# Optimization experiments

Hardware: AMD Instinct MI355X
Metric: run time of the kernel (lower is better)

Reference implementation:

```python
import jax, jax.numpy as jnp
import numpy as np

N_RAYS = 8192
N_SURF = 2048
EPS = 1e-18  # matches torch zero-denominator patch value


def setup_inputs() -> dict:
    key = jax.random.key(0)
    k1, k2, k3 = jax.random.split(key, 3)
    o = jax.random.normal(k1, (N_RAYS, 3), dtype=jnp.float32)
    d = jax.random.normal(k2, (N_RAYS, 3), dtype=jnp.float32)
    V = jax.random.normal(k3, (N_SURF, 4, 3), dtype=jnp.float32)
    return {"o": o, "d": d, "V": V}


def _safe(x):
    # torch code sets exact-zero denominators to 1e-18 via nonzero() indexing
    return jnp.where(x == 0.0, EPS, x)


def reference(o, d, V):
    # --- get_intersections: ray-plane intersection scalars t (N, M) ---
    v = jnp.cross(V[:, 1] - V[:, 0], V[:, 2] - V[:, 0])          # (M,3) plane normals
    v = v / jnp.linalg.norm(v, axis=1, keepdims=True)
    k = -jnp.sum(v * V[:, 3], axis=1)                             # (M,) plane offsets
    vo = o @ v.T                                                  # (N,M)
    vd = d @ v.T                                                  # (N,M)
    t = -(k[None, :] + vo) / vd                                   # (N,M)

    # intersection points r = o + t*d, broadcast over surfaces -> (N,M,3)
    r = o[:, None, :] + t[..., None] * d[:, None, :]

    # --- get_onsurface_surface_intersections: barycentric masking ---
    a = V[None, :, 0]  # (1,M,3) broadcast instead of .repeat
    b = V[None, :, 1]
    c = V[None, :, 2]
    ax, ay, az = a[..., 0], a[..., 1], a[..., 2]
    rx, ry, rz = r[..., 0], r[..., 1], r[..., 2]

    A = ax * rz - az * rx
    B = ax * b[..., 2] - az * b[..., 0]
    C = ax * ry - ay * rx
    D = ax * b[..., 1] - ay * b[..., 0]
    E = ax * c[..., 2] - az * c[..., 0]
    F = B * (ay * c[..., 0] - ax * c[..., 1])
    G = D

    gam = (G * (A * D - B * C)) / _safe(D * (E * G + F))          # (N,M)
    beta = (C + gam * (ay * c[..., 0] - ax * c[..., 1])) / _safe(D)
    alpha = (rx - (beta * b[..., 0] + gam * c[..., 0])) / _safe(ax)

    mask = (beta > 0.0) & (gam > 0.0) & (alpha > 0.0)             # (N,M) bool
    return t * mask.astype(t.dtype)                               # masked intersection depths
```

## Files before the change

### kernel.cpp

```cpp
#include <hip/hip_runtime.h>


#define N_RAYS 8192
#define N_SURF 2048
constexpr int RPB = 16;
constexpr int SPT = 2;

typedef float v2f __attribute__((ext_vector_type(2)));
#define FMA2(a, b, c) __builtin_elementwise_fma((a), (b), (c))

__device__ __forceinline__ float safef(float x) {
    return (x == 0.0f) ? 1e-18f : x;
}

__global__ __launch_bounds__(256) void coeff_kernel(
    const float* __restrict__ V, float* __restrict__ cf)
{
    const int s = blockIdx.x * 256 + threadIdx.x;

    const float4 p0 = *(const float4*)(V + (size_t)s * 12);
    const float4 p1 = *(const float4*)(V + (size_t)s * 12 + 4);
    const float4 p2 = *(const float4*)(V + (size_t)s * 12 + 8);
    const float ax = p0.x, ay = p0.y, az = p0.z;
    const float bx = p0.w, by = p1.x, bz = p1.y;
    const float cx = p1.z, cy = p1.w, cz = p2.x;
    const float wx = p2.y, wy = p2.z, wz = p2.w;

    const float e0x = bx - ax, e0y = by - ay, e0z = bz - az;
    const float e1x = cx - ax, e1y = cy - ay, e1z = cz - az;
    const float nx = e0y * e1z - e0z * e1y;
    const float ny = e0z * e1x - e0x * e1z;
    const float nz = e0x * e1y - e0y * e1x;
    const float rn = __builtin_amdgcn_rsqf(fmaf(nx, nx, fmaf(ny, ny, nz * nz)));
    const float vx = nx * rn, vy = ny * rn, vz = nz * rn;
    const float k = -fmaf(vx, wx, fmaf(vy, wy, vz * wz));

    const float B  = ax * bz - az * bx;
    const float D  = ax * by - ay * bx;
    const float E  = ax * cz - az * cx;
    const float P  = ay * cx - ax * cy;
    const float F  = B * P;
    const float rden = __builtin_amdgcn_rcpf(safef(D * fmaf(E, D, F)));
    const float rD   = __builtin_amdgcn_rcpf(safef(D));
    const float rAX  = __builtin_amdgcn_rcpf(safef(ax));

    const float DB = D * B, DD = D * D;
    const float g0 = (DB * ay - DD * az) * rden;
    const float g1 = -(DB * ax) * rden;
    const float g2 = (DD * ax) * rden;
    const float bp  = P * rD;
    const float bb0 = fmaf(bp, g0, -ay * rD);
    const float bb1 = fmaf(bp, g1,  ax * rD);
    const float bb2 = bp * g2;
    const float ab = -bx * rAX, ac = -cx * rAX;
    const float aa0 = fmaf(ab, bb0, fmaf(ac, g0, rAX));
    const float aa1 = fmaf(ab, bb1, ac * g1);
    const float aa2 = fmaf(ab, bb2, ac * g2);

    cf[ 0 * N_SURF + s] = vx;
    cf[ 1 * N_SURF + s] = vy;
    cf[ 2 * N_SURF + s] = vz;
    cf[ 3 * N_SURF + s] = k;
    cf[ 4 * N_SURF + s] = g0;
    cf[ 5 * N_SURF + s] = g1;
    cf[ 6 * N_SURF + s] = g2;
    cf[ 7 * N_SURF + s] = bb0;
    cf[ 8 * N_SURF + s] = bb1;
    cf[ 9 * N_SURF + s] = bb2;
    cf[10 * N_SURF + s] = aa0;
    cf[11 * N_SURF + s] = aa1;
    cf[12 * N_SURF + s] = aa2;
}

__global__ __launch_bounds__(256, 8) void trace_kernel(
    const float* __restrict__ o, const float* __restrict__ dr,
    const float* __restrict__ cf, float* __restrict__ out)
{
    const int s0 = (blockIdx.x * 256 + threadIdx.x) * SPT;

    const v2f vx  = *(const v2f*)(cf +  0 * N_SURF + s0);
    const v2f vy  = *(const v2f*)(cf +  1 * N_SURF + s0);
    const v2f vz  = *(const v2f*)(cf +  2 * N_SURF + s0);
    const v2f kk  = *(const v2f*)(cf +  3 * N_SURF + s0);
    const v2f g0  = *(const v2f*)(cf +  4 * N_SURF + s0);
    const v2f g1  = *(const v2f*)(cf +  5 * N_SURF + s0);
    const v2f g2  = *(const v2f*)(cf +  6 * N_SURF + s0);
    const v2f bb0 = *(const v2f*)(cf +  7 * N_SURF + s0);
    const v2f bb1 = *(const v2f*)(cf +  8 * N_SURF + s0);
    const v2f bb2 = *(const v2f*)(cf +  9 * N_SURF + s0);
    const v2f aa0 = *(const v2f*)(cf + 10 * N_SURF + s0);
    const v2f aa1 = *(const v2f*)(cf + 11 * N_SURF + s0);
    const v2f aa2 = *(const v2f*)(cf + 12 * N_SURF + s0);

    const int ray0 = blockIdx.y * RPB;
    float* outp = out + (size_t)ray0 * N_SURF + s0;

#pragma unroll 4
    for (int i = 0; i < RPB; ++i) {
        const int ray = ray0 + i;
        const float o0 = o[ray * 3 + 0], o1 = o[ray * 3 + 1], o2 = o[ray * 3 + 2];
        const float d0 = dr[ray * 3 + 0], d1 = dr[ray * 3 + 1], d2 = dr[ray * 3 + 2];
        const v2f o0v = o0, o1v = o1, o2v = o2;
        const v2f d0v = d0, d1v = d1, d2v = d2;

        const v2f vo_k = FMA2(o0v, vx, FMA2(o1v, vy, FMA2(o2v, vz, kk)));
        const v2f vd   = FMA2(d0v, vx, FMA2(d1v, vy, d2v * vz));
        v2f rv;
        rv.x = __builtin_amdgcn_rcpf(vd.x);
        rv.y = __builtin_amdgcn_rcpf(vd.y);
        const v2f t = -vo_k * rv;

        const v2f rx = FMA2(t, d0v, o0v);
        const v2f ry = FMA2(t, d1v, o1v);
        const v2f rz = FMA2(t, d2v, o2v);

        const v2f gam = FMA2(g0,  rx, FMA2(g1,  ry, g2  * rz));
        const v2f bet = FMA2(bb0, rx, FMA2(bb1, ry, bb2 * rz));
        const v2f alp = FMA2(aa0, rx, FMA2(aa1, ry, aa2 * rz));

        const float mnx = fminf(fminf(bet.x, gam.x), alp.x);
        const float mny = fminf(fminf(bet.y, gam.y), alp.y);
        v2f res;
        res.x = (mnx > 0.0f) ? t.x : 0.0f;
        res.y = (mny > 0.0f) ? t.y : 0.0f;
        *(v2f*)(outp + (size_t)i * N_SURF) = res;
    }
}

extern "C" void kernel_launch(void* const* d_in, const int* in_sizes, int n_in,
                              void* d_out, int out_size, void* d_ws, size_t ws_size,
                              hipStream_t stream) {
    const float* o  = (const float*)d_in[0];
    const float* dr = (const float*)d_in[1];
    const float* V  = (const float*)d_in[2];
    float* out = (float*)d_out;
    float* cf  = (float*)d_ws;

    coeff_kernel<<<dim3(N_SURF / 256), dim3(256), 0, stream>>>(V, cf);
    trace_kernel<<<dim3(N_SURF / (256 * SPT), N_RAYS / RPB), dim3(256), 0, stream>>>(o, dr, cf, out);
}
```

Before: 86.20 us.

## Fuse per-surface coefficient computation into trace kernel, one launch

Removes the separate coefficient kernel and its workspace round-trip. Each thread in the trace kernel now recomputes the 13 coefficients for its two surfaces directly from V. Blocks grow to 1024 threads covering all surfaces, and each block handles 32 rays. This saves a kernel launch and the dependency between the two kernels. The cost is redundant coefficient math in every block (256 times over) and a different grid shape.

```diff
diff --git a/kernel.cpp b/kernel.cpp
--- a/kernel.cpp
+++ b/kernel.cpp
@@ -3,8 +3,9 @@
 
 #define N_RAYS 8192
 #define N_SURF 2048
-constexpr int RPB = 16;
+constexpr int RPB = 32;
 constexpr int SPT = 2;
+constexpr int TPB = 1024;
 
 typedef float v2f __attribute__((ext_vector_type(2)));
 #define FMA2(a, b, c) __builtin_elementwise_fma((a), (b), (c))
@@ -13,11 +14,9 @@
     return (x == 0.0f) ? 1e-18f : x;
 }
 
-__global__ __launch_bounds__(256) void coeff_kernel(
-    const float* __restrict__ V, float* __restrict__ cf)
+__device__ __forceinline__ void surf_coeffs(const float* __restrict__ V, int s,
+                                            float* __restrict__ c)
 {
-    const int s = blockIdx.x * 256 + threadIdx.x;
-
     const float4 p0 = *(const float4*)(V + (size_t)s * 12);
     const float4 p1 = *(const float4*)(V + (size_t)s * 12 + 4);
     const float4 p2 = *(const float4*)(V + (size_t)s * 12 + 8);
@@ -57,42 +56,36 @@
     const float aa1 = fmaf(ab, bb1, ac * g1);
     const float aa2 = fmaf(ab, bb2, ac * g2);
 
-    cf[ 0 * N_SURF + s] = vx;
-    cf[ 1 * N_SURF + s] = vy;
-    cf[ 2 * N_SURF + s] = vz;
-    cf[ 3 * N_SURF + s] = k;
-    cf[ 4 * N_SURF + s] = g0;
-    cf[ 5 * N_SURF + s] = g1;
-    cf[ 6 * N_SURF + s] = g2;
-    cf[ 7 * N_SURF + s] = bb0;
-    cf[ 8 * N_SURF + s] = bb1;
-    cf[ 9 * N_SURF + s] = bb2;
-    cf[10 * N_SURF + s] = aa0;
-    cf[11 * N_SURF + s] = aa1;
-    cf[12 * N_SURF + s] = aa2;
+    c[0] = vx;  c[1] = vy;  c[2] = vz;  c[3] = k;
+    c[4] = g0;  c[5] = g1;  c[6] = g2;
+    c[7] = bb0; c[8] = bb1; c[9] = bb2;
+    c[10] = aa0; c[11] = aa1; c[12] = aa2;
 }
 
-__global__ __launch_bounds__(256, 8) void trace_kernel(
+__global__ __launch_bounds__(TPB, 4) void trace_kernel(
     const float* __restrict__ o, const float* __restrict__ dr,
-    const float* __restrict__ cf, float* __restrict__ out)
+    const float* __restrict__ V, float* __restrict__ out)
 {
-    const int s0 = (blockIdx.x * 256 + threadIdx.x) * SPT;
+    const int s0 = threadIdx.x * SPT;
 
-    const v2f vx  = *(const v2f*)(cf +  0 * N_SURF + s0);
-    const v2f vy  = *(const v2f*)(cf +  1 * N_SURF + s0);
-    const v2f vz  = *(const v2f*)(cf +  2 * N_SURF + s0);
-    const v2f kk  = *(const v2f*)(cf +  3 * N_SURF + s0);
-    const v2f g0  = *(const v2f*)(cf +  4 * N_SURF + s0);
-    const v2f g1  = *(const v2f*)(cf +  5 * N_SURF + s0);
-    const v2f g2  = *(const v2f*)(cf +  6 * N_SURF + s0);
-    const v2f bb0 = *(const v2f*)(cf +  7 * N_SURF + s0);
-    const v2f bb1 = *(const v2f*)(cf +  8 * N_SURF + s0);
-    const v2f bb2 = *(const v2f*)(cf +  9 * N_SURF + s0);
-    const v2f aa0 = *(const v2f*)(cf + 10 * N_SURF + s0);
-    const v2f aa1 = *(const v2f*)(cf + 11 * N_SURF + s0);
-    const v2f aa2 = *(const v2f*)(cf + 12 * N_SURF + s0);
+    float cA[13], cB[13];
+    surf_coeffs(V, s0, cA);
+    surf_coeffs(V, s0 + 1, cB);
+    const v2f vx  = {cA[0],  cB[0]};
+    const v2f vy  = {cA[1],  cB[1]};
+    const v2f vz  = {cA[2],  cB[2]};
+    const v2f kk  = {cA[3],  cB[3]};
+    const v2f g0  = {cA[4],  cB[4]};
+    const v2f g1  = {cA[5],  cB[5]};
+    const v2f g2  = {cA[6],  cB[6]};
+    const v2f bb0 = {cA[7],  cB[7]};
+    const v2f bb1 = {cA[8],  cB[8]};
+    const v2f bb2 = {cA[9],  cB[9]};
+    const v2f aa0 = {cA[10], cB[10]};
+    const v2f aa1 = {cA[11], cB[11]};
+    const v2f aa2 = {cA[12], cB[12]};
 
-    const int ray0 = blockIdx.y * RPB;
+    const int ray0 = blockIdx.x * RPB;
     float* outp = out + (size_t)ray0 * N_SURF + s0;
 
 #pragma unroll 4
@@ -134,8 +127,6 @@
     const float* dr = (const float*)d_in[1];
     const float* V  = (const float*)d_in[2];
     float* out = (float*)d_out;
-    float* cf  = (float*)d_ws;
 
-    coeff_kernel<<<dim3(N_SURF / 256), dim3(256), 0, stream>>>(V, cf);
-    trace_kernel<<<dim3(N_SURF / (256 * SPT), N_RAYS / RPB), dim3(256), 0, stream>>>(o, dr, cf, out);
+    trace_kernel<<<dim3(N_RAYS / RPB), dim3(TPB), 0, stream>>>(o, dr, V, out);
 }
```

After: 85.41 us. Within noise of the previous version (-0.9%).
